# Optimization experiments

Measured on AMD Instinct MI355X. Metric: run time of the kernel, lower is better.

The kernel has to match this reference:

```python
import jax, jax.numpy as jnp
import numpy as np

B, S, T = 16, 400, 51
V, E, H = 50000, 128, 256
MAX_OOV = 50
EXT = V + MAX_OOV
COV_LOSS_WEIGHT = 1.0


def setup_inputs() -> dict:
    key = jax.random.key(0)
    ks = jax.random.split(key, 24)
    sc = 0.05  # param scale
    inp = {
        "tgt": jax.random.randint(ks[0], (B, T), 0, V, dtype=jnp.int32),
        "hidden": jax.random.normal(ks[1], (1, B, H), jnp.float32),
        "cell": jax.random.normal(ks[2], (1, B, H), jnp.float32),
        "encoder_outputs": jax.random.normal(ks[3], (B, S, H), jnp.float32),
        "src_lens": jax.random.randint(ks[4], (B,), S // 2, S + 1, dtype=jnp.int32),
        "src_ids": jax.random.randint(ks[5], (B, S), 0, V, dtype=jnp.int32),
        # -1 means in-vocab token; >=0 means OOV slot index (max MAX_OOV-1)
        "src_oov_map": jax.random.randint(ks[6], (B, S), -1, MAX_OOV, dtype=jnp.int32),
        "embedding": jax.random.normal(ks[7], (V, E), jnp.float32) * sc,
        "W_h": jax.random.normal(ks[8], (H, H), jnp.float32) * sc,
        "W_s": jax.random.normal(ks[9], (H, H), jnp.float32) * sc,
        "w_c": jax.random.normal(ks[10], (H,), jnp.float32) * sc,
        "v": jax.random.normal(ks[11], (H,), jnp.float32) * sc,
        "b_attn": jnp.zeros((1,), jnp.float32),
        "W_ih": jax.random.normal(ks[12], (4 * H, E + H), jnp.float32) * sc,
        "W_hh": jax.random.normal(ks[13], (4 * H, H), jnp.float32) * sc,
        "b_ih": jax.random.normal(ks[14], (4 * H,), jnp.float32) * sc,
        "b_hh": jax.random.normal(ks[15], (4 * H,), jnp.float32) * sc,
        "W_pg": jax.random.normal(ks[16], (1, 2 * H + E), jnp.float32) * sc,
        "b_pg": jnp.zeros((1,), jnp.float32),
        "W_out": jax.random.normal(ks[17], (V, 2 * H), jnp.float32) * sc,
        "b_out": jnp.zeros((V,), jnp.float32),
    }
    return inp


def reference(tgt, hidden, cell, encoder_outputs, src_lens, src_ids, src_oov_map,
              embedding, W_h, W_s, w_c, v, b_attn,
              W_ih, W_hh, b_ih, b_hh, W_pg, b_pg, W_out, b_out):
    # Precompute encoder projection and masks (loop-invariant)
    Wh_h = jnp.einsum('bsh,kh->bsk', encoder_outputs, W_h)        # [B,S,H]
    pad_mask = jnp.arange(S)[None, :] >= src_lens[:, None]       # [B,S]
    copy_idx = jnp.where(src_oov_map >= 0, V + src_oov_map, src_ids)  # [B,S]
    batch_idx = jnp.arange(B)[:, None]

    def step(carry, y_prev):
        h, c, cov = carry                                       # [B,H],[B,H],[B,S]
        emb = embedding[y_prev]                                 # [B,E]
        # coverage attention (additive, See et al. 2017 eq. 9-11)
        attn_in = Wh_h + (h @ W_s.T)[:, None, :] + cov[..., None] * w_c + b_attn
        scores = jnp.tanh(attn_in) @ v                          # [B,S]
        scores = jnp.where(pad_mask, -1e9, scores)
        attn = jax.nn.softmax(scores, axis=1)                   # [B,S]
        context = jnp.einsum('bs,bsh->bh', attn, encoder_outputs)
        cov_loss = jnp.sum(jnp.minimum(attn, cov), axis=1)      # [B]
        # single-layer LSTM cell (torch gate order i,f,g,o)
        x = jnp.concatenate([emb, context], axis=1)             # [B,E+H]
        gates = x @ W_ih.T + h @ W_hh.T + b_ih + b_hh
        i, f, g, o = jnp.split(gates, 4, axis=1)
        c_new = jax.nn.sigmoid(f) * c + jax.nn.sigmoid(i) * jnp.tanh(g)
        h_new = jax.nn.sigmoid(o) * jnp.tanh(c_new)
        # pointer-generator mixture
        p_gen = jax.nn.sigmoid(
            jnp.concatenate([h_new, context, emb], axis=1) @ W_pg.T + b_pg)  # [B,1]
        logits = jnp.concatenate([h_new, context], axis=1) @ W_out.T + b_out
        vocab_dist = jax.nn.softmax(logits, axis=1)             # [B,V]
        ext_dist = jnp.pad(vocab_dist, ((0, 0), (0, MAX_OOV)))  # [B,EXT]
        copy_dist = jnp.zeros((B, EXT), vocab_dist.dtype).at[batch_idx, copy_idx].add(attn)
        final = p_gen * ext_dist + (1.0 - p_gen) * copy_dist
        return (h_new, c_new, cov + attn), (final, cov_loss)

    carry0 = (hidden[0], cell[0], jnp.zeros((B, S), jnp.float32))
    # teacher forcing: decoder input at step t is tgt[:, t-1], t = 1..T-1
    (hT, cT, _), (dists, cov_losses) = jax.lax.scan(step, carry0, tgt[:, :-1].T)
    all_dists = jnp.transpose(dists, (1, 0, 2))                 # [B,T-1,EXT]
    coverage_loss = COV_LOSS_WEIGHT * jnp.mean(cov_losses)
    return all_dists, hT[None], cT[None], coverage_loss
```

## Files before the change

kernel.cpp:

```cpp
#include <hip/hip_runtime.h>
#include <math.h>

#define CB 16
#define CS 400
#define CT 51
#define CTM1 50
#define CV 50000
#define CE 128
#define CH 256
#define CMAXOOV 50
#define CEXT (CV + CMAXOOV)
#define CX 640
#define NST 16
#define NGT 16
#define NWK 223
#define NBLK 256
#define NTILE 782

typedef __attribute__((ext_vector_type(4))) float f32x4;
typedef __attribute__((ext_vector_type(8))) short short8;
typedef unsigned int U32;
typedef unsigned long long U64;

__device__ __forceinline__ float wave_sum(float x) {
#pragma unroll
  for (int o = 32; o > 0; o >>= 1) x += __shfl_xor(x, o);
  return x;
}
__device__ __forceinline__ float sigm(float x) {
  return 1.f / (1.f + __expf(-x));
}
__device__ __forceinline__ float ftanh(float x) {
  x = fminf(fmaxf(x, -15.f), 15.f);
  float e = __expf(2.f * x);
  return (e - 1.f) / (e + 1.f);
}
__device__ __forceinline__ unsigned short f2bf(float f) {
  union { float f; U32 u; } x;
  x.f = f;
  U32 r = x.u + 0x7FFFu + ((x.u >> 16) & 1u);
  return (unsigned short)(r >> 16);
}
__device__ __forceinline__ float bf2f(unsigned short u) {
  return __uint_as_float(((U32)u) << 16);
}
__device__ __forceinline__ U64 pack4(float a, float b, float c, float d) {
  return (U64)f2bf(a) | ((U64)f2bf(b) << 16) | ((U64)f2bf(c) << 32) |
         ((U64)f2bf(d) << 48);
}
__device__ __forceinline__ U32 ald32(const U32* p) {
  return __hip_atomic_load(p, __ATOMIC_RELAXED, __HIP_MEMORY_SCOPE_AGENT);
}
__device__ __forceinline__ void ast32(U32* p, U32 v) {
  __hip_atomic_store(p, v, __ATOMIC_RELAXED, __HIP_MEMORY_SCOPE_AGENT);
}
__device__ __forceinline__ void astf(float* p, float v) {
  __hip_atomic_store((U32*)p, __float_as_uint(v), __ATOMIC_RELAXED,
                     __HIP_MEMORY_SCOPE_AGENT);
}
__device__ __forceinline__ void ast64(U64* p, U64 v) {
  __hip_atomic_store(p, v, __ATOMIC_RELAXED, __HIP_MEMORY_SCOPE_AGENT);
}
#define VM0 asm volatile("s_waitcnt vmcnt(0)" ::: "memory")

__global__ __launch_bounds__(256) void pw_convert(
    const float* __restrict__ W, unsigned short* __restrict__ Wb) {
  size_t i = ((size_t)blockIdx.x * 256 + threadIdx.x) * 8;
  float4 a = *(const float4*)(W + i);
  float4 b = *(const float4*)(W + i + 4);
  short8 o;
  o[0] = (short)f2bf(a.x); o[1] = (short)f2bf(a.y);
  o[2] = (short)f2bf(a.z); o[3] = (short)f2bf(a.w);
  o[4] = (short)f2bf(b.x); o[5] = (short)f2bf(b.y);
  o[6] = (short)f2bf(b.z); o[7] = (short)f2bf(b.w);
  *(short8*)(Wb + i) = o;
}

__global__ __launch_bounds__(256) void pw_cat(
    const float* __restrict__ W_ih, const float* __restrict__ W_hh,
    unsigned short* __restrict__ Wcat) {
  int t8 = blockIdx.x * 256 + threadIdx.x;
  int j = t8 / 80, k8 = t8 % 80;
  short8 o;
#pragma unroll
  for (int i = 0; i < 8; ++i) {
    int k = k8 * 8 + i;
    float v = (k < CE + CH) ? W_ih[(size_t)j * (CE + CH) + k]
                            : W_hh[(size_t)j * CH + (k - (CE + CH))];
    o[i] = (short)f2bf(v);
  }
  *(short8*)(Wcat + (size_t)t8 * 8) = o;
}

__global__ __launch_bounds__(256) void pw_t256(const float* __restrict__ in,
                                               float* __restrict__ out) {
  int j = blockIdx.x, k = threadIdx.x;
  out[j * CH + k] = in[k * CH + j];
}

__global__ __launch_bounds__(256) void pw_t256_bf16(
    const float* __restrict__ in, unsigned short* __restrict__ out) {
  int j = blockIdx.x, k = threadIdx.x;
  out[j * CH + k] = f2bf(in[k * CH + j]);
}

__global__ __launch_bounds__(256) void pw_cvt16(
    const float* __restrict__ in, unsigned short* __restrict__ out) {
  size_t i = ((size_t)blockIdx.x * 256 + threadIdx.x) * 8;
  float4 a = *(const float4*)(in + i);
  float4 b = *(const float4*)(in + i + 4);
  short8 o;
  o[0] = (short)f2bf(a.x); o[1] = (short)f2bf(a.y);
  o[2] = (short)f2bf(a.z); o[3] = (short)f2bf(a.w);
  o[4] = (short)f2bf(b.x); o[5] = (short)f2bf(b.y);
  o[6] = (short)f2bf(b.z); o[7] = (short)f2bf(b.w);
  *(short8*)(out + i) = o;
}

__global__ __launch_bounds__(256) void p0_precompute(
    const float* __restrict__ enc, const float* __restrict__ W_hT,
    const int* __restrict__ src_ids, const int* __restrict__ src_oov,
    unsigned short* __restrict__ Wh_h16, int* __restrict__ copy_idx) {
  const int row0 = blockIdx.x * 8, tid = threadIdx.x;
  __shared__ float erT[CH * 8];
#pragma unroll
  for (int i = 0; i < 8; ++i) {
    int idx = tid + i * 256;
    int r = idx >> 8, j = idx & 255;
    erT[j * 8 + r] = enc[(size_t)row0 * CH + idx];
  }
  if (tid < 8) {
    int row = row0 + tid;
    int ov = src_oov[row];
    copy_idx[row] = (ov >= 0) ? (CV + ov) : src_ids[row];
  }
  __syncthreads();
  float acc[8] = {0, 0, 0, 0, 0, 0, 0, 0};
#pragma unroll 4
  for (int j = 0; j < CH; ++j) {
    float w = W_hT[j * CH + tid];
    float4 e0 = *(const float4*)&erT[j * 8];
    float4 e1 = *(const float4*)&erT[j * 8 + 4];
    acc[0] += e0.x * w; acc[1] += e0.y * w; acc[2] += e0.z * w; acc[3] += e0.w * w;
    acc[4] += e1.x * w; acc[5] += e1.y * w; acc[6] += e1.z * w; acc[7] += e1.w * w;
  }
#pragma unroll
  for (int r = 0; r < 8; ++r)
    Wh_h16[(size_t)(row0 + r) * CH + tid] = f2bf(acc[r]);
}

__global__ __launch_bounds__(256) void z_init(U32* __restrict__ ctrl,
                                              float* __restrict__ part) {
  int tid = blockIdx.x * 256 + threadIdx.x;
  if (tid < 2048) ctrl[tid] = 0u;
  for (int i = tid; i < CTM1 * CB * 64; i += 256 * 64) part[i] = 0.f;
}

__global__ __launch_bounds__(1024, 4) void mega(
    const int* __restrict__ tgt, const float* __restrict__ hidden,
    const float* __restrict__ cell, const int* __restrict__ src_lens,
    const float* __restrict__ embedding, const float* __restrict__ w_c,
    const float* __restrict__ v_vec, const float* __restrict__ b_attn,
    const float* __restrict__ b_ih, const float* __restrict__ b_hh,
    const float* __restrict__ W_pg, const float* __restrict__ b_pg,
    const float* __restrict__ b_out,
    const unsigned short* __restrict__ Wh_h16,
    const unsigned short* __restrict__ enc16,
    const unsigned short* __restrict__ W_sT16,
    const unsigned short* __restrict__ Wcat,
    const unsigned short* __restrict__ Wb, U64* __restrict__ A64,
    float* __restrict__ HexF, float* __restrict__ HwsP,
    float* __restrict__ PgP, unsigned short* __restrict__ attn16,
    float* __restrict__ p_gen_g, float* __restrict__ part,
    float* __restrict__ covloss_b, U32* __restrict__ ctrl,
    float* __restrict__ dout) {
  const int bid = blockIdx.x, tid = threadIdx.x;
  const int lane = tid & 63, wv = tid >> 6;
  U32* release = ctrl + 256;
  U32* xrdy = ctrl + 1280;
  U32* grdy = ctrl + 1536;

  __shared__ __align__(16) U64 sh_big[2592];
  __shared__ float cov_s[CS];
  __shared__ float a_s[CS];
  __shared__ __align__(16) float h_cur[CH];
  __shared__ float hws_s[CH];
  __shared__ __align__(16) float ctx_s[CH];
  __shared__ float emb_s[CE];
  __shared__ float pctx[4 * CH];
  __shared__ float gsl[4][4][64];
  __shared__ int sh_tok[CB];
  __shared__ float red[16];
  __shared__ float stat[4];
  __shared__ float prs[16][16];

  if (bid < NST) {
    const int b = bid;
    const int gi = b >> 2;
    const int len = src_lens[b];
    const float ba = b_attn[0];
    const int k4 = lane * 4;
    const float4 wc4 = *(const float4*)(w_c + k4);
    const float4 vv4 = *(const float4*)(v_vec + k4);
    const int kg = tid & 255, grp = tid >> 8;
    float covl = 0.f;

    if (tid < CS) cov_s[tid] = 0.f;
    if (tid < CH) h_cur[tid] = hidden[b * CH + tid];
    __syncthreads();
    {
      float acc = 0.f;
#pragma unroll 8
      for (int j = grp * 64; j < grp * 64 + 64; ++j)
        acc += h_cur[j] * bf2f(W_sT16[j * CH + kg]);
      pctx[grp * CH + kg] = acc;
    }
    __syncthreads();
    if (tid < CH)
      hws_s[tid] = pctx[tid] + pctx[CH + tid] + pctx[2 * CH + tid] +
                   pctx[3 * CH + tid];
    __syncthreads();

    for (int t = 0; t < CTM1; ++t) {
      if (t > 0) {
        if (tid < CS) {
          float a = a_s[tid], cv = cov_s[tid];
          covl += fminf(a, cv);
          cov_s[tid] = cv + a;
        }
        __syncthreads();
      }
      float ps = 0.f;
      for (int s = wv; s < CS; s += 16) {
        float cv = cov_s[s];
        U64 wq = *(const U64*)(Wh_h16 + ((size_t)(b * CS + s)) * CH + k4);
        float p =
            ftanh(bf2f((unsigned short)wq) + hws_s[k4] + cv * wc4.x + ba) *
                vv4.x +
            ftanh(bf2f((unsigned short)(wq >> 16)) + hws_s[k4 + 1] +
                  cv * wc4.y + ba) *
                vv4.y +
            ftanh(bf2f((unsigned short)(wq >> 32)) + hws_s[k4 + 2] +
                  cv * wc4.z + ba) *
                vv4.z +
            ftanh(bf2f((unsigned short)(wq >> 48)) + hws_s[k4 + 3] +
                  cv * wc4.w + ba) *
                vv4.w;
        p = wave_sum(p);
        if (lane == 0) {
          float e = (s < len) ? __expf(p) : 0.f;
          a_s[s] = e;
          ps += e;
        }
      }
      if (lane == 0) red[wv] = ps;
      __syncthreads();
      if (tid == 0) {
        float s2 = 0.f;
#pragma unroll
        for (int i = 0; i < 16; ++i) s2 += red[i];
        stat[0] = 1.f / s2;
      }
      __syncthreads();
      const float inv = stat[0];
      if (tid < CS) {
        float a = a_s[tid] * inv;
        a_s[tid] = a;
        attn16[((size_t)t * CB + b) * CS + tid] = f2bf(a);
      }
      __syncthreads();
      {
        float pc = 0.f;
        const unsigned short* er =
            enc16 + ((size_t)(b * CS + grp * 100)) * CH + kg;
#pragma unroll 10
        for (int i = 0; i < 100; ++i)
          pc += a_s[grp * 100 + i] * bf2f(er[(size_t)i * CH]);
        pctx[grp * CH + kg] = pc;
      }
      __syncthreads();
      if (tid < CH)
        ctx_s[tid] = pctx[tid] + pctx[CH + tid] + pctx[2 * CH + tid] +
                     pctx[3 * CH + tid];
      if (tid < CE)
        emb_s[tid] = embedding[(size_t)tgt[b * CT + t] * CE + tid];
      __syncthreads();
      if (tid < 64) {
        ast64(&A64[(size_t)t * 2048 + b * 128 + 64 + tid],
              pack4(ctx_s[4 * tid], ctx_s[4 * tid + 1], ctx_s[4 * tid + 2],
                    ctx_s[4 * tid + 3]));
      }
      VM0;
      __syncthreads();
      if (tid == 0) ast32(&xrdy[b * 16], (U32)(t + 1));
      {
        float z = 0.f;
        if (tid < CH) z = ctx_s[tid] * W_pg[CH + tid];
        if (tid < CE) z += emb_s[tid] * W_pg[2 * CH + tid];
        z = wave_sum(z);
        if (lane == 0) red[wv] = z;
      }
      __syncthreads();
      if (wv == 0) {
        int gg = 0;
        while (gg < (1 << 22)) {
          U32 v = (lane < 4) ? ald32(&grdy[(gi * 4 + lane) * 16])
                             : (U32)(t + 1);
          if (__all(v >= (U32)(t + 1))) break;
          __builtin_amdgcn_s_sleep(1);
          ++gg;
        }
      }
      __syncthreads();
      if (tid < CH) {
        const float* hp = HwsP + (((size_t)t * CB + b) * 4) * CH + tid;
        hws_s[tid] = hp[0] + hp[CH] + hp[2 * CH] + hp[3 * CH];
      }
      if (tid == 0) {
        float s2 = 0.f;
#pragma unroll
        for (int i = 0; i < 16; ++i) s2 += red[i];
        const float* pp = PgP + ((size_t)t * CB + b) * 4;
        s2 += pp[0] + pp[1] + pp[2] + pp[3];
        p_gen_g[t * CB + b] = sigm(s2 + b_pg[0]);
      }
      __syncthreads();
    }
    if (tid < CS) covl += fminf(a_s[tid], cov_s[tid]);
    covl = wave_sum(covl);
    if (lane == 0) red[wv] = covl;
    __syncthreads();
    if (tid == 0) {
      float s2 = 0.f;
#pragma unroll
      for (int i = 0; i < 16; ++i) s2 += red[i];
      covloss_b[b] = s2;
    }
    if (tid < CH) {
      const size_t D0 = (size_t)CB * CTM1 * CEXT;
      dout[D0 + b * CH + tid] = HexF[((size_t)49 * CB + b) * CH + tid];
    }
  } else if (bid < NST + NGT) {
    const int g = bid - NST;
    const int gi = g >> 2, gj = g & 3;
    const int b0 = gi * 4, u0 = gj * 64;
    const int nn = lane & 15, gq = lane >> 4;
    U64* xg64 = sh_big;
    short* xg_s = (short*)sh_big;
    const short8* x8 = (const short8*)sh_big;
    const int g2 = wv >> 2;
    const int ncol = g2 * 256 + u0 + (wv & 3) * 16 + nn;
    const short8* bp = (const short8*)Wcat + (size_t)ncol * 80;
    const int cbL = wv, cu = lane;
    float c_reg = 0.f, bi0 = 0.f, bi1 = 0.f, bi2 = 0.f, bi3 = 0.f;
    if (wv < 4) {
      c_reg = cell[(b0 + cbL) * CH + u0 + cu];
      bi0 = b_ih[u0 + cu] + b_hh[u0 + cu];
      bi1 = b_ih[CH + u0 + cu] + b_hh[CH + u0 + cu];
      bi2 = b_ih[2 * CH + u0 + cu] + b_hh[2 * CH + u0 + cu];
      bi3 = b_ih[3 * CH + u0 + cu] + b_hh[3 * CH + u0 + cu];
    }
    for (int t = 0; t < CTM1; ++t) {
      if (t > 0 && wv == 0) {
        int gg = 0;
        while (gg < (1 << 22)) {
          U32 v = (lane < 4) ? ald32(&grdy[(gi * 4 + lane) * 16]) : (U32)t;
          if (__all(v >= (U32)t)) break;
          __builtin_amdgcn_s_sleep(1);
          ++gg;
        }
      }
      if (tid < 4) sh_tok[tid] = tgt[(b0 + tid) * CT + t];
      __syncthreads();
      if (tid < 512) {
        int bb = tid >> 7, k = tid & 127;
        xg_s[bb * 648 + k] =
            (short)f2bf(embedding[(size_t)sh_tok[bb] * CE + k]);
      }
      if (t == 0) {
        if (tid < 1024) {
          int bb = tid >> 8, k = tid & 255;
          xg_s[bb * 648 + 384 + k] = (short)f2bf(hidden[(b0 + bb) * CH + k]);
        }
      } else {
        if (tid < 256) {
          int bb = tid >> 6, iu = tid & 63;
          xg64[bb * 162 + 96 + iu] =
              A64[(size_t)(t - 1) * 2048 + (b0 + bb) * 128 + iu];
        }
      }
      __syncthreads();
      f32x4 acc = {0.f, 0.f, 0.f, 0.f};
      {
#pragma unroll
        for (int kt = 0; kt < 4; ++kt)
          acc = __builtin_amdgcn_mfma_f32_16x16x32_bf16(
              x8[nn * 81 + kt * 4 + gq], bp[kt * 4 + gq], acc, 0, 0, 0);
#pragma unroll
        for (int kt = 12; kt < 20; ++kt)
          acc = __builtin_amdgcn_mfma_f32_16x16x32_bf16(
              x8[nn * 81 + kt * 4 + gq], bp[kt * 4 + gq], acc, 0, 0, 0);
      }
      if (wv == 0) {
        int gg = 0;
        while (gg < (1 << 22)) {
          U32 v = (lane < 4) ? ald32(&xrdy[(b0 + lane) * 16]) : (U32)(t + 1);
          if (__all(v >= (U32)(t + 1))) break;
          __builtin_amdgcn_s_sleep(1);
          ++gg;
        }
      }
      __syncthreads();
      if (tid < 256) {
        int bb = tid >> 6, iu = tid & 63;
        xg64[bb * 162 + 32 + iu] =
            A64[(size_t)t * 2048 + (b0 + bb) * 128 + 64 + iu];
      }
      __syncthreads();
      {
#pragma unroll
        for (int kt = 4; kt < 12; ++kt)
          acc = __builtin_amdgcn_mfma_f32_16x16x32_bf16(
              x8[nn * 81 + kt * 4 + gq], bp[kt * 4 + gq], acc, 0, 0, 0);
        if (gq == 0) {
#pragma unroll
          for (int r = 0; r < 4; ++r)
            gsl[g2][r][(wv & 3) * 16 + nn] = acc[r];
        }
      }
      __syncthreads();
      if (wv < 4) {
        float gi_ = gsl[0][cbL][cu] + bi0;
        float gf = gsl[1][cbL][cu] + bi1;
        float gg2 = gsl[2][cbL][cu] + bi2;
        float go = gsl[3][cbL][cu] + bi3;
        float cn = sigm(gf) * c_reg + sigm(gi_) * ftanh(gg2);
        c_reg = cn;
        float hn = sigm(go) * ftanh(cn);
        h_cur[cbL * 64 + cu] = hn;
        astf(&HexF[((size_t)t * CB + b0 + cbL) * CH + u0 + cu], hn);
        float h1 = __shfl_down(hn, 1);
        float h2 = __shfl_down(hn, 2);
        float h3 = __shfl_down(hn, 3);
        if (!(cu & 3))
          ast64(&A64[(size_t)t * 2048 + (b0 + cbL) * 128 + gj * 16 +
                     (cu >> 2)],
                pack4(hn, h1, h2, h3));
      }
      __syncthreads();
      {
        int bb = tid >> 8, k = tid & 255;
        float acc2 = 0.f;
#pragma unroll 8
        for (int u = 0; u < 64; ++u)
          acc2 += h_cur[bb * 64 + u] * bf2f(W_sT16[(u0 + u) * CH + k]);
        astf(&HwsP[(((size_t)t * CB + b0 + bb) * 4 + gj) * CH + k], acc2);
      }
      if (wv < 4) {
        float pp = h_cur[cbL * 64 + cu] * W_pg[u0 + cu];
        pp = wave_sum(pp);
        if (cu == 0)
          astf(&PgP[((size_t)t * CB + b0 + cbL) * 4 + gj], pp);
      }
      VM0;
      __syncthreads();
      if (tid == 0) ast32(&grdy[g * 16], (U32)(t + 1));
    }
    if (wv < 4) {
      const size_t D0 = (size_t)CB * CTM1 * CEXT;
      dout[D0 + CB * CH + (b0 + cbL) * CH + u0 + cu] = c_reg;
    }
  } else if (bid == NST + NGT) {
    for (int t = 0; t < CTM1; ++t) {
      if (wv == 0) {
        int gg = 0;
        while (gg < (1 << 22)) {
          U32 v = (lane < NGT) ? ald32(&grdy[lane * 16]) : (U32)(t + 1);
          if (__all(v >= (U32)(t + 1))) break;
          __builtin_amdgcn_s_sleep(4);
          ++gg;
        }
      }
      __syncthreads();
      if (tid < 64) ast32(&release[tid * 16], (U32)(t + 1));
      __syncthreads();
    }
  } else {
    const int vb = bid - NST - NGT - 1;
    const int rep = vb & 63;
    const int nn = lane & 15, g = lane >> 4;
    const int t4 = (wv >> 2) * NWK + vb;
    const int v = t4 * 64 + (wv & 3) * 16 + nn;
    const bool live = (t4 < NTILE) && (v < CV);
    const int vc = live ? v : CV - 1;
    U64* a64l = sh_big;
    const short8* lds8 = (const short8*)sh_big;
    const short8* bp = (const short8*)Wb + (size_t)vc * 64;
    const float bo = live ? b_out[v] : 0.f;
    for (int t = 0; t < CTM1; ++t) {
      if (tid == 0) {
        int gg = 0;
        while (ald32(&release[rep * 16]) < (U32)(t + 1) && ++gg < (1 << 18))
          __builtin_amdgcn_s_sleep(32);
      }
      __syncthreads();
      {
        const U64* src = A64 + (size_t)t * 2048;
#pragma unroll
        for (int i = 0; i < 2; ++i) {
          int idx = tid + i * 1024;
          int row = idx >> 7, col = idx & 127;
          a64l[row * 130 + col] = src[idx];
        }
      }
      __syncthreads();
      short8 af[16];
#pragma unroll
      for (int kt = 0; kt < 16; ++kt) af[kt] = lds8[nn * 65 + kt * 4 + g];
      f32x4 acc = {0.f, 0.f, 0.f, 0.f};
#pragma unroll
      for (int kt = 0; kt < 16; ++kt)
        acc = __builtin_amdgcn_mfma_f32_16x16x32_bf16(af[kt], bp[kt * 4 + g],
                                                      acc, 0, 0, 0);
      float ev[4];
#pragma unroll
      for (int r = 0; r < 4; ++r) {
        float e = live ? __expf(acc[r] + bo) : 0.f;
        if (live) dout[((size_t)((g * 4 + r) * CTM1 + t)) * CEXT + v] = e;
#pragma unroll
        for (int o = 1; o < 16; o <<= 1) e += __shfl_xor(e, o);
        ev[r] = e;
      }
      if (nn == 0) {
#pragma unroll
        for (int r = 0; r < 4; ++r) prs[wv][g * 4 + r] = ev[r];
      }
      __syncthreads();
      if (tid < 16) {
        float s = 0.f;
#pragma unroll
        for (int w = 0; w < 16; ++w) s += prs[w][tid];
        atomicAdd(&part[((size_t)t * CB + tid) * 64 + rep], s);
      }
      __syncthreads();
    }
  }
}

__global__ __launch_bounds__(256) void post_norm(
    const float* __restrict__ part, const float* __restrict__ p_gen_g,
    float* __restrict__ dout) {
  const int R = blockIdx.x;
  const int b = R / CTM1, t = R % CTM1;
  const int tid = threadIdx.x;
  __shared__ float stat;
  float s = (tid < 64) ? part[((size_t)t * CB + b) * 64 + tid] : 0.f;
  s = wave_sum(s);
  if (tid == 0) stat = p_gen_g[t * CB + b] / s;
  __syncthreads();
  float inv = stat;
  float* drow = dout + (size_t)R * CEXT;
  for (int v = tid; v < CEXT; v += 256)
    drow[v] = (v < CV) ? drow[v] * inv : 0.f;
}

__global__ __launch_bounds__(256) void post_tail(
    const unsigned short* __restrict__ attn16,
    const float* __restrict__ p_gen_g, const int* __restrict__ copy_idx,
    const float* __restrict__ covloss_b, float* __restrict__ dout) {
  const int b = blockIdx.x, tid = threadIdx.x;
  for (int t = 0; t < CTM1; ++t) {
    float pg1 = 1.f - p_gen_g[t * CB + b];
    const unsigned short* ar = attn16 + ((size_t)t * CB + b) * CS;
    float* drow = dout + ((size_t)(b * CTM1 + t)) * CEXT;
    for (int s = tid; s < CS; s += 256)
      atomicAdd(drow + copy_idx[b * CS + s], pg1 * bf2f(ar[s]));
  }
  if (b == 0 && tid == 0) {
    const size_t D0 = (size_t)CB * CTM1 * CEXT;
    float s = 0.f;
    for (int i = 0; i < CB; ++i) s += covloss_b[i];
    dout[D0 + 2 * CB * CH] = s / (float)(CTM1 * CB);
  }
}

extern "C" void kernel_launch(void* const* d_in, const int* in_sizes, int n_in,
                              void* d_out, int out_size, void* d_ws,
                              size_t ws_size, hipStream_t stream) {
  const int* tgt = (const int*)d_in[0];
  const float* hidden = (const float*)d_in[1];
  const float* cell = (const float*)d_in[2];
  const float* enc = (const float*)d_in[3];
  const int* src_lens = (const int*)d_in[4];
  const int* src_ids = (const int*)d_in[5];
  const int* src_oov = (const int*)d_in[6];
  const float* embedding = (const float*)d_in[7];
  const float* W_h = (const float*)d_in[8];
  const float* W_s = (const float*)d_in[9];
  const float* w_c = (const float*)d_in[10];
  const float* v_vec = (const float*)d_in[11];
  const float* b_attn = (const float*)d_in[12];
  const float* W_ih = (const float*)d_in[13];
  const float* W_hh = (const float*)d_in[14];
  const float* b_ih = (const float*)d_in[15];
  const float* b_hh = (const float*)d_in[16];
  const float* W_pg = (const float*)d_in[17];
  const float* b_pg = (const float*)d_in[18];
  const float* W_out = (const float*)d_in[19];
  const float* b_out = (const float*)d_in[20];
  float* dout = (float*)d_out;

  float* ws = (float*)d_ws;
  float* W_hT = ws;
  float* p_gen_g = W_hT + CH * CH;
  float* part = p_gen_g + CTM1 * CB;
  float* covloss_b = part + CTM1 * CB * 64;
  float* HexF = covloss_b + 16;
  float* HwsP = HexF + (size_t)CTM1 * CB * CH;
  float* PgP = HwsP + (size_t)CTM1 * CB * 4 * CH;
  int* copy_idx = (int*)(PgP + CTM1 * CB * 4);
  U32* ctrl = (U32*)(copy_idx + CB * CS);
  U64* A64 = (U64*)(ctrl + 2048);
  unsigned short* attn16 =
      (unsigned short*)(A64 + (size_t)CTM1 * 2048);
  unsigned short* Wh_h16 = attn16 + (size_t)CTM1 * CB * CS;
  unsigned short* enc16 = Wh_h16 + (size_t)CB * CS * CH;
  unsigned short* W_sT16 = enc16 + (size_t)CB * CS * CH;
  unsigned short* Wcat = W_sT16 + CH * CH;
  unsigned short* Wb = Wcat + (size_t)(4 * CH) * CX;

  z_init<<<64, 256, 0, stream>>>(ctrl, part);
  pw_convert<<<(CV * 2 * CH) / (256 * 8), 256, 0, stream>>>(W_out, Wb);
  pw_cat<<<((4 * CH) * CX / 8) / 256, 256, 0, stream>>>(W_ih, W_hh, Wcat);
  pw_t256<<<CH, CH, 0, stream>>>(W_h, W_hT);
  pw_t256_bf16<<<CH, CH, 0, stream>>>(W_s, W_sT16);
  pw_cvt16<<<(CB * CS * CH) / (256 * 8), 256, 0, stream>>>(enc, enc16);
  p0_precompute<<<CB * CS / 8, 256, 0, stream>>>(enc, W_hT, src_ids, src_oov,
                                                 Wh_h16, copy_idx);

  void* kargs[] = {
      (void*)&tgt,      (void*)&hidden,    (void*)&cell,    (void*)&src_lens,
      (void*)&embedding,(void*)&w_c,       (void*)&v_vec,   (void*)&b_attn,
      (void*)&b_ih,     (void*)&b_hh,      (void*)&W_pg,    (void*)&b_pg,
      (void*)&b_out,    (void*)&Wh_h16,    (void*)&enc16,   (void*)&W_sT16,
      (void*)&Wcat,     (void*)&Wb,        (void*)&A64,     (void*)&HexF,
      (void*)&HwsP,     (void*)&PgP,       (void*)&attn16,  (void*)&p_gen_g,
      (void*)&part,     (void*)&covloss_b, (void*)&ctrl,    (void*)&dout};
  hipError_t e = hipLaunchCooperativeKernel((const void*)mega, dim3(NBLK),
                                            dim3(1024), kargs, 0, stream);
  if (e != hipSuccess) {
    hipLaunchKernelGGL(mega, dim3(NBLK), dim3(1024), 0, stream, tgt, hidden,
                       cell, src_lens, embedding, w_c, v_vec, b_attn, b_ih,
                       b_hh, W_pg, b_pg, b_out, Wh_h16, enc16, W_sT16, Wcat,
                       Wb, A64, HexF, HwsP, PgP, attn16, p_gen_g, part,
                       covloss_b, ctrl, dout);
  }
  post_norm<<<CB * CTM1, 256, 0, stream>>>(part, p_gen_g, dout);
  post_tail<<<CB, 256, 0, stream>>>(attn16, p_gen_g, copy_idx, covloss_b,
                                    dout);
}
```

Baseline: 2.105 ms.

## Move W_s projection and p_gen into attention blocks; skip padded source positions

The gate blocks no longer compute partial h·W_s products, p_gen partials, or the fp32 hidden-state export through global scratch. Instead each attention block reads the bf16-packed new hidden state from A64 and computes the full W_s projection and p_gen itself. The attention score and context loops now stop at src_len instead of running over all 400 positions, and the unused scratch buffers are removed. This cuts cross-block global traffic and padded work, but it puts a 256x256 matvec on the attention block's critical path and uses a bf16-rounded h for the projection and p_gen, which may shift numerics.

```diff
diff --git a/kernel.cpp b/kernel.cpp
--- a/kernel.cpp
+++ b/kernel.cpp
@@ -51,12 +51,11 @@
 __device__ __forceinline__ U32 ald32(const U32* p) {
   return __hip_atomic_load(p, __ATOMIC_RELAXED, __HIP_MEMORY_SCOPE_AGENT);
 }
+__device__ __forceinline__ U64 ald64(const U64* p) {
+  return __hip_atomic_load(p, __ATOMIC_RELAXED, __HIP_MEMORY_SCOPE_AGENT);
+}
 __device__ __forceinline__ void ast32(U32* p, U32 v) {
   __hip_atomic_store(p, v, __ATOMIC_RELAXED, __HIP_MEMORY_SCOPE_AGENT);
-}
-__device__ __forceinline__ void astf(float* p, float v) {
-  __hip_atomic_store((U32*)p, __float_as_uint(v), __ATOMIC_RELAXED,
-                     __HIP_MEMORY_SCOPE_AGENT);
 }
 __device__ __forceinline__ void ast64(U64* p, U64 v) {
   __hip_atomic_store(p, v, __ATOMIC_RELAXED, __HIP_MEMORY_SCOPE_AGENT);
@@ -169,11 +168,9 @@
     const unsigned short* __restrict__ W_sT16,
     const unsigned short* __restrict__ Wcat,
     const unsigned short* __restrict__ Wb, U64* __restrict__ A64,
-    float* __restrict__ HexF, float* __restrict__ HwsP,
-    float* __restrict__ PgP, unsigned short* __restrict__ attn16,
-    float* __restrict__ p_gen_g, float* __restrict__ part,
-    float* __restrict__ covloss_b, U32* __restrict__ ctrl,
-    float* __restrict__ dout) {
+    unsigned short* __restrict__ attn16, float* __restrict__ p_gen_g,
+    float* __restrict__ part, float* __restrict__ covloss_b,
+    U32* __restrict__ ctrl, float* __restrict__ dout) {
   const int bid = blockIdx.x, tid = threadIdx.x;
   const int lane = tid & 63, wv = tid >> 6;
   U32* release = ctrl + 256;
@@ -205,7 +202,7 @@
     const int kg = tid & 255, grp = tid >> 8;
     float covl = 0.f;
 
-    if (tid < CS) cov_s[tid] = 0.f;
+    if (tid < CS) { cov_s[tid] = 0.f; a_s[tid] = 0.f; }
     if (tid < CH) h_cur[tid] = hidden[b * CH + tid];
     __syncthreads();
     {
@@ -231,7 +228,7 @@
         __syncthreads();
       }
       float ps = 0.f;
-      for (int s = wv; s < CS; s += 16) {
+      for (int s = wv; s < len; s += 16) {
         float cv = cov_s[s];
         U64 wq = *(const U64*)(Wh_h16 + ((size_t)(b * CS + s)) * CH + k4);
         float p =
@@ -248,7 +245,7 @@
                 vv4.w;
         p = wave_sum(p);
         if (lane == 0) {
-          float e = (s < len) ? __expf(p) : 0.f;
+          float e = __expf(p);
           a_s[s] = e;
           ps += e;
         }
@@ -271,10 +268,11 @@
       __syncthreads();
       {
         float pc = 0.f;
+        int hi = len - grp * 100;
+        hi = (hi < 0) ? 0 : ((hi > 100) ? 100 : hi);
         const unsigned short* er =
             enc16 + ((size_t)(b * CS + grp * 100)) * CH + kg;
-#pragma unroll 10
-        for (int i = 0; i < 100; ++i)
+        for (int i = 0; i < hi; ++i)
           pc += a_s[grp * 100 + i] * bf2f(er[(size_t)i * CH]);
         pctx[grp * CH + kg] = pc;
       }
@@ -293,14 +291,6 @@
       VM0;
       __syncthreads();
       if (tid == 0) ast32(&xrdy[b * 16], (U32)(t + 1));
-      {
-        float z = 0.f;
-        if (tid < CH) z = ctx_s[tid] * W_pg[CH + tid];
-        if (tid < CE) z += emb_s[tid] * W_pg[2 * CH + tid];
-        z = wave_sum(z);
-        if (lane == 0) red[wv] = z;
-      }
-      __syncthreads();
       if (wv == 0) {
         int gg = 0;
         while (gg < (1 << 22)) {
@@ -312,17 +302,39 @@
         }
       }
       __syncthreads();
-      if (tid < CH) {
-        const float* hp = HwsP + (((size_t)t * CB + b) * 4) * CH + tid;
-        hws_s[tid] = hp[0] + hp[CH] + hp[2 * CH] + hp[3 * CH];
-      }
-      if (tid == 0) {
-        float s2 = 0.f;
-#pragma unroll
-        for (int i = 0; i < 16; ++i) s2 += red[i];
-        const float* pp = PgP + ((size_t)t * CB + b) * 4;
-        s2 += pp[0] + pp[1] + pp[2] + pp[3];
-        p_gen_g[t * CB + b] = sigm(s2 + b_pg[0]);
+      if (tid < 64) {
+        U64 v = ald64(&A64[(size_t)t * 2048 + b * 128 + tid]);
+        h_cur[4 * tid] = bf2f((unsigned short)v);
+        h_cur[4 * tid + 1] = bf2f((unsigned short)(v >> 16));
+        h_cur[4 * tid + 2] = bf2f((unsigned short)(v >> 32));
+        h_cur[4 * tid + 3] = bf2f((unsigned short)(v >> 48));
+      }
+      __syncthreads();
+      {
+        float acc = 0.f;
+#pragma unroll 8
+        for (int j = grp * 64; j < grp * 64 + 64; ++j)
+          acc += h_cur[j] * bf2f(W_sT16[j * CH + kg]);
+        pctx[grp * CH + kg] = acc;
+      }
+      __syncthreads();
+      if (tid < CH)
+        hws_s[tid] = pctx[tid] + pctx[CH + tid] + pctx[2 * CH + tid] +
+                     pctx[3 * CH + tid];
+      {
+        float z = 0.f;
+        if (tid < CH)
+          z = h_cur[tid] * W_pg[tid] + ctx_s[tid] * W_pg[CH + tid];
+        if (tid < CE) z += emb_s[tid] * W_pg[2 * CH + tid];
+        z = wave_sum(z);
+        if (lane == 0) red[wv] = z;
+        __syncthreads();
+        if (tid == 0) {
+          float s2 = 0.f;
+#pragma unroll
+          for (int i = 0; i < 16; ++i) s2 += red[i];
+          p_gen_g[t * CB + b] = sigm(s2 + b_pg[0]);
+        }
       }
       __syncthreads();
     }
@@ -335,10 +347,6 @@
 #pragma unroll
       for (int i = 0; i < 16; ++i) s2 += red[i];
       covloss_b[b] = s2;
-    }
-    if (tid < CH) {
-      const size_t D0 = (size_t)CB * CTM1 * CEXT;
-      dout[D0 + b * CH + tid] = HexF[((size_t)49 * CB + b) * CH + tid];
     }
   } else if (bid < NST + NGT) {
     const int g = bid - NST;
@@ -386,7 +394,7 @@
         if (tid < 256) {
           int bb = tid >> 6, iu = tid & 63;
           xg64[bb * 162 + 96 + iu] =
-              A64[(size_t)(t - 1) * 2048 + (b0 + bb) * 128 + iu];
+              ald64(&A64[(size_t)(t - 1) * 2048 + (b0 + bb) * 128 + iu]);
         }
       }
       __syncthreads();
@@ -414,7 +422,7 @@
       if (tid < 256) {
         int bb = tid >> 6, iu = tid & 63;
         xg64[bb * 162 + 32 + iu] =
-            A64[(size_t)t * 2048 + (b0 + bb) * 128 + 64 + iu];
+            ald64(&A64[(size_t)t * 2048 + (b0 + bb) * 128 + 64 + iu]);
       }
       __syncthreads();
       {
@@ -437,8 +445,10 @@
         float cn = sigm(gf) * c_reg + sigm(gi_) * ftanh(gg2);
         c_reg = cn;
         float hn = sigm(go) * ftanh(cn);
-        h_cur[cbL * 64 + cu] = hn;
-        astf(&HexF[((size_t)t * CB + b0 + cbL) * CH + u0 + cu], hn);
+        if (t == CTM1 - 1) {
+          const size_t D0 = (size_t)CB * CTM1 * CEXT;
+          dout[D0 + (b0 + cbL) * CH + u0 + cu] = hn;
+        }
         float h1 = __shfl_down(hn, 1);
         float h2 = __shfl_down(hn, 2);
         float h3 = __shfl_down(hn, 3);
@@ -446,21 +456,6 @@
           ast64(&A64[(size_t)t * 2048 + (b0 + cbL) * 128 + gj * 16 +
                      (cu >> 2)],
                 pack4(hn, h1, h2, h3));
-      }
-      __syncthreads();
-      {
-        int bb = tid >> 8, k = tid & 255;
-        float acc2 = 0.f;
-#pragma unroll 8
-        for (int u = 0; u < 64; ++u)
-          acc2 += h_cur[bb * 64 + u] * bf2f(W_sT16[(u0 + u) * CH + k]);
-        astf(&HwsP[(((size_t)t * CB + b0 + bb) * 4 + gj) * CH + k], acc2);
-      }
-      if (wv < 4) {
-        float pp = h_cur[cbL * 64 + cu] * W_pg[u0 + cu];
-        pp = wave_sum(pp);
-        if (cu == 0)
-          astf(&PgP[((size_t)t * CB + b0 + cbL) * 4 + gj], pp);
       }
       VM0;
       __syncthreads();
@@ -615,10 +610,7 @@
   float* p_gen_g = W_hT + CH * CH;
   float* part = p_gen_g + CTM1 * CB;
   float* covloss_b = part + CTM1 * CB * 64;
-  float* HexF = covloss_b + 16;
-  float* HwsP = HexF + (size_t)CTM1 * CB * CH;
-  float* PgP = HwsP + (size_t)CTM1 * CB * 4 * CH;
-  int* copy_idx = (int*)(PgP + CTM1 * CB * 4);
+  int* copy_idx = (int*)(covloss_b + 16);
   U32* ctrl = (U32*)(copy_idx + CB * CS);
   U64* A64 = (U64*)(ctrl + 2048);
   unsigned short* attn16 =
@@ -643,17 +635,16 @@
       (void*)&embedding,(void*)&w_c,       (void*)&v_vec,   (void*)&b_attn,
       (void*)&b_ih,     (void*)&b_hh,      (void*)&W_pg,    (void*)&b_pg,
       (void*)&b_out,    (void*)&Wh_h16,    (void*)&enc16,   (void*)&W_sT16,
-      (void*)&Wcat,     (void*)&Wb,        (void*)&A64,     (void*)&HexF,
-      (void*)&HwsP,     (void*)&PgP,       (void*)&attn16,  (void*)&p_gen_g,
-      (void*)&part,     (void*)&covloss_b, (void*)&ctrl,    (void*)&dout};
+      (void*)&Wcat,     (void*)&Wb,        (void*)&A64,     (void*)&attn16,
+      (void*)&p_gen_g,  (void*)&part,      (void*)&covloss_b,(void*)&ctrl,
+      (void*)&dout};
   hipError_t e = hipLaunchCooperativeKernel((const void*)mega, dim3(NBLK),
                                             dim3(1024), kargs, 0, stream);
   if (e != hipSuccess) {
     hipLaunchKernelGGL(mega, dim3(NBLK), dim3(1024), 0, stream, tgt, hidden,
                        cell, src_lens, embedding, w_c, v_vec, b_attn, b_ih,
                        b_hh, W_pg, b_pg, b_out, Wh_h16, enc16, W_sT16, Wcat,
-                       Wb, A64, HexF, HwsP, PgP, attn16, p_gen_g, part,
-                       covloss_b, ctrl, dout);
+                       Wb, A64, attn16, p_gen_g, part, covloss_b, ctrl, dout);
   }
   post_norm<<<CB * CTM1, 256, 0, stream>>>(part, p_gen_g, dout);
   post_tail<<<CB, 256, 0, stream>>>(attn16, p_gen_g, copy_idx, covloss_b,
```

Measured after the change: 1.776 ms. 15.7% less time.
